# Performance work log

Hardware: AMD Instinct MI355X
Metric: run time of the kernel (lower is better)

The kernel has to match this reference:

```python
import jax, jax.numpy as jnp
import numpy as np
from jax import lax

NUM_CLASSES = 3
NORMALIZE = True
INF = 1e6  # finite 'infinity'; INF**2 = 1e12 is safely representable in fp32


def _dist_along_axis0(m):
    """Per-column 1D distance to nearest True along axis 0. m: [H,W] bool -> [H,W] float."""
    W = m.shape[1]
    init = jnp.full((W,), INF, dtype=jnp.float32)

    def step(carry, row):
        d = jnp.where(row, 0.0, carry + 1.0)
        return d, d

    _, fwd = lax.scan(step, init, m)
    _, bwd = lax.scan(step, init, m[::-1])
    return jnp.minimum(fwd, bwd[::-1])


def _dist_to_set(m):
    """Exact Euclidean distance to nearest True pixel (separable EDT). m: [H,W] bool."""
    W = m.shape[1]
    g = _dist_along_axis0(m)  # [H,W]: min |i-i'| with m[i',j]
    j = jnp.arange(W, dtype=jnp.float32)
    offs = (j[:, None] - j[None, :]) ** 2  # [W_out, W_src]
    # D2[i,j] = min_k g[i,k]^2 + (j-k)^2  (exact 2D squared EDT)
    d2 = jnp.min(g[:, None, :] ** 2 + offs[None, :, :], axis=-1)  # [H,W]
    return jnp.sqrt(d2)


def _sdf(mask):
    """Signed distance map bg_dist - fg_dist for one binary mask [H,W], matching onehot_to_sdf."""
    fg_dist = _dist_to_set(~mask)  # scipy edt(fg): distance to nearest zero of fg
    bg_dist = _dist_to_set(mask)   # scipy edt(1-fg): distance to nearest fg pixel
    if NORMALIZE:
        fg_dist = fg_dist / jnp.maximum(jnp.max(fg_dist), 1e-12)
        bg_dist = bg_dist / jnp.maximum(jnp.max(bg_dist), 1e-12)
    return jnp.where(jnp.any(mask), bg_dist - fg_dist, 0.0)


def _distance_maps(targets):
    onehot = jax.nn.one_hot(targets, NUM_CLASSES, axis=-1) > 0.5  # [B,H,W,C] bool
    masks = jnp.moveaxis(onehot, -1, 1)  # [B,C,H,W]
    B, C, H, W = masks.shape
    maps = lax.map(_sdf, masks.reshape(B * C, H, W))  # sequential: bounds peak memory
    return maps.reshape(B, C, H, W)


def setup_inputs() -> dict:
    key = jax.random.key(0)
    k1, k2 = jax.random.split(key)
    logits = jax.random.normal(k1, (8, 3, 384, 384), dtype=jnp.float32)
    targets = jax.random.randint(k2, (8, 384, 384), 0, 3, dtype=jnp.int32)
    return {"logits": logits, "targets": targets}


def reference(logits, targets):
    probs = jax.nn.softmax(logits, axis=1)              # [B,C,H,W]
    dist_maps = _distance_maps(targets)                  # [B,C,H,W]
    per_class = jnp.mean(probs * dist_maps, axis=(0, 2, 3))  # mean over b,h,w
    return jnp.mean(per_class)  # class_weights=None -> plain mean over classes
```

## Files before the change

### kernel.cpp

```cpp
#include <hip/hip_runtime.h>

typedef unsigned long long u64;
typedef unsigned short u16;

#define HH 384
#define WW 384
#define BB 8
#define CC 3
#define NMASK (BB*CC)
#define PLANE (HH*WW)
#define NW 6
#define ROWS_PG 4
#define GROUPS 96
#define CHUNK 4
#define INF_F 1.0e6f


template <int CTRL>
__device__ __forceinline__ float dpp_mov(float v) {
    return __int_as_float(__builtin_amdgcn_update_dpp(
        0, __float_as_int(v), CTRL, 0xf, 0xf, true));
}
__device__ __forceinline__ float wave_sum64(float v) {
    v += dpp_mov<0x111>(v);
    v += dpp_mov<0x112>(v);
    v += dpp_mov<0x114>(v);
    v += dpp_mov<0x118>(v);
    v += dpp_mov<0x142>(v);
    v += dpp_mov<0x143>(v);
    return v;
}
__device__ __forceinline__ float wave_max64(float v) {
    v = fmaxf(v, dpp_mov<0x111>(v));
    v = fmaxf(v, dpp_mov<0x112>(v));
    v = fmaxf(v, dpp_mov<0x114>(v));
    v = fmaxf(v, dpp_mov<0x118>(v));
    v = fmaxf(v, dpp_mov<0x142>(v));
    v = fmaxf(v, dpp_mov<0x143>(v));
    return v;
}

__global__ __launch_bounds__(WW) void buildbm(const int* __restrict__ targets,
                                              u16* __restrict__ bm16) {
    int b = blockIdx.x, w = blockIdx.y, q = blockIdx.z;
    int j = threadIdx.x;
    const int* tg = targets + (size_t)b * PLANE + (w * 64 + q * 16) * WW + j;
    int t[16];
#pragma unroll
    for (int r = 0; r < 16; ++r) t[r] = tg[r * WW];
    unsigned m0 = 0, m1 = 0, m2 = 0;
#pragma unroll
    for (int r = 0; r < 16; ++r) {
        unsigned bit = 1u << r;
        m0 |= (t[r] == 0) ? bit : 0u;
        m1 |= (t[r] == 1) ? bit : 0u;
        m2 |= (t[r] == 2) ? bit : 0u;
    }
    size_t base = (((size_t)b * CC) * NW + w) * WW + j;
    bm16[base * 4 + q] = (u16)m0;
    bm16[(base + (size_t)NW * WW) * 4 + q] = (u16)m1;
    bm16[(base + 2 * (size_t)NW * WW) * 4 + q] = (u16)m2;
}

__global__ __launch_bounds__(WW, 5) void edt4w(const u64* __restrict__ bm,
                                               const float* __restrict__ logits,
                                               float* __restrict__ out12) {
    __shared__ __align__(16) float g2s[ROWS_PG][CC][WW];
    __shared__ float red[12][WW / 64];
    int g = blockIdx.x, b = blockIdx.y;
    int j = threadIdx.x;
    int i0 = g * ROWS_PG;
    int w = i0 >> 6;
    int wbase = w << 6;

    u64 wb[CC][NW];
#pragma unroll
    for (int c = 0; c < CC; ++c)
#pragma unroll
        for (int wq = 0; wq < NW; ++wq)
            wb[c][wq] = bm[(((size_t)b * CC + c) * NW + wq) * WW + j];

    const float* lg = logits + ((size_t)b * CC * HH + i0) * WW + j;
    float lv[ROWS_PG][CC];
#pragma unroll
    for (int rl = 0; rl < ROWS_PG; ++rl) {
        lv[rl][0] = lg[rl * WW];
        lv[rl][1] = lg[PLANE + rl * WW];
        lv[rl][2] = lg[2 * PLANE + rl * WW];
    }

    u64 word[CC];
    int P[CC], N[CC];
#pragma unroll
    for (int c = 0; c < CC; ++c) {
        int p = -1, n = -1;
#pragma unroll
        for (int wq = 0; wq < NW; ++wq)
            if (wq < w && wb[c][wq]) p = wq * 64 + 63 - __builtin_clzll(wb[c][wq] | 1ull);
#pragma unroll
        for (int wq = NW - 1; wq >= 0; --wq)
            if (wq > w && wb[c][wq]) n = wq * 64 + (int)__builtin_ctzll(wb[c][wq] | 0x8000000000000000ull);
        P[c] = p; N[c] = n;
        u64 wd = wb[c][0];
#pragma unroll
        for (int wq = 1; wq < NW; ++wq) wd = (w == wq) ? wb[c][wq] : wd;
        word[c] = wd;
    }

    u64 lowmask = ((1ull << (i0 & 63)) << 1) - 1ull;
#pragma unroll
    for (int rl = 0; rl < ROWS_PG; ++rl) {
        int i = i0 + rl;
        u64 himask = ~(lowmask >> 1);
#pragma unroll
        for (int c = 0; c < CC; ++c) {
            u64 lo = word[c] & lowmask;
            int last = lo ? (wbase + 63 - __builtin_clzll(lo | 1ull)) : P[c];
            u64 hi = word[c] & himask;
            int next = hi ? (wbase + (int)__builtin_ctzll(hi | 0x8000000000000000ull)) : N[c];
            float fwd = (last >= 0) ? (float)(i - last) : (INF_F + (float)(i + 1));
            float bwd = (next >= 0) ? (float)(next - i) : (INF_F + (float)(HH - i));
            float gc = fminf(fwd, bwd);
            g2s[rl][c][j] = gc * gc;
        }
        lowmask = (lowmask << 1) | 1ull;
    }
    __syncthreads();

    int basek = (j - 4) & ~3;
    if (basek < 0) basek = 0;
    if (basek > WW - 12) basek = WW - 12;
    float df0 = (float)(basek - j);

    float Sb0 = 0.f, Sb1 = 0.f, Sb2 = 0.f, Sf0 = 0.f, Sf1 = 0.f, Sf2 = 0.f;
    float Mb0 = 0.f, Mb1 = 0.f, Mb2 = 0.f, Mf0 = 0.f, Mf1 = 0.f, Mf2 = 0.f;
#pragma unroll
    for (int rl = 0; rl < ROWS_PG; ++rl) {
        int bi = (i0 + rl) & 63;
        float l0 = lv[rl][0], l1 = lv[rl][1], l2 = lv[rl][2];
        float mx = fmaxf(l0, fmaxf(l1, l2));
        float x0 = __expf(l0 - mx), x1 = __expf(l1 - mx), x2 = __expf(l2 - mx);
        float rs = __fdividef(1.0f, x0 + x1 + x2);
        float pr0 = x0 * rs, pr1 = x1 * rs, pr2 = x2 * rs;

        float d[CC];
#pragma unroll
        for (int c = 0; c < CC; ++c) {
            const float* g2 = g2s[rl][c];
            float4 W0 = *(const float4*)(g2 + basek);
            float4 W1 = *(const float4*)(g2 + basek + 4);
            float4 W2 = *(const float4*)(g2 + basek + 8);
            float df = df0;
            float mn;
            mn =           fmaf(df, df, W0.x);  df += 1.f;
            mn = fminf(mn, fmaf(df, df, W0.y)); df += 1.f;
            mn = fminf(mn, fmaf(df, df, W0.z)); df += 1.f;
            mn = fminf(mn, fmaf(df, df, W0.w)); df += 1.f;
            mn = fminf(mn, fmaf(df, df, W1.x)); df += 1.f;
            mn = fminf(mn, fmaf(df, df, W1.y)); df += 1.f;
            mn = fminf(mn, fmaf(df, df, W1.z)); df += 1.f;
            mn = fminf(mn, fmaf(df, df, W1.w)); df += 1.f;
            mn = fminf(mn, fmaf(df, df, W2.x)); df += 1.f;
            mn = fminf(mn, fmaf(df, df, W2.y)); df += 1.f;
            mn = fminf(mn, fmaf(df, df, W2.z)); df += 1.f;
            mn = fminf(mn, fmaf(df, df, W2.w));
            if (mn > 25.f) {
                for (int r0 = 5; r0 < WW; r0 += CHUNK) {
                    float r0sq = (float)(r0 * r0);
                    if (r0sq >= mn) break;
                    float cl[CHUNK], cr[CHUNK];
#pragma unroll
                    for (int u = 0; u < CHUNK; ++u) {
                        int r = r0 + u;
                        int kl = j - r; kl = (kl < 0) ? 0 : kl;
                        int kr = j + r; kr = (kr > WW - 1) ? WW - 1 : kr;
                        cl[u] = g2[kl];
                        cr[u] = g2[kr];
                    }
#pragma unroll
                    for (int u = 0; u < CHUNK; ++u) {
                        float rr = (float)((r0 + u) * (r0 + u));
                        mn = fminf(mn, fminf(rr + cl[u], rr + cr[u]));
                    }
                }
            }
            d[c] = sqrtf(mn);
        }
        float f0 = ((word[0] >> bi) & 1ull) ? fminf(d[1], d[2]) : 0.f;
        float f1 = ((word[1] >> bi) & 1ull) ? fminf(d[0], d[2]) : 0.f;
        float f2 = ((word[2] >> bi) & 1ull) ? fminf(d[0], d[1]) : 0.f;

        Sb0 += pr0 * d[0]; Sb1 += pr1 * d[1]; Sb2 += pr2 * d[2];
        Sf0 += pr0 * f0;   Sf1 += pr1 * f1;   Sf2 += pr2 * f2;
        Mb0 = fmaxf(Mb0, d[0]); Mb1 = fmaxf(Mb1, d[1]); Mb2 = fmaxf(Mb2, d[2]);
        Mf0 = fmaxf(Mf0, f0);   Mf1 = fmaxf(Mf1, f1);   Mf2 = fmaxf(Mf2, f2);
    }

    float acc[12] = {Sb0, Sf0, Mb0, Mf0, Sb1, Sf1, Mb1, Mf1, Sb2, Sf2, Mb2, Mf2};
    int lane = j & 63, wid = j >> 6;
#pragma unroll
    for (int a = 0; a < 12; ++a) {
        bool ismax = (a & 2) != 0;
        float v = ismax ? wave_max64(acc[a]) : wave_sum64(acc[a]);
        if (lane == 63) red[a][wid] = v;
    }
    __syncthreads();
    if (j < 12) {
        int c = j >> 2, k = j & 3;
        bool ismax = (k & 2) != 0;
        float v = red[j][0];
#pragma unroll
        for (int t = 1; t < WW / 64; ++t)
            v = ismax ? fmaxf(v, red[j][t]) : (v + red[j][t]);
        out12[((size_t)(b * CC + c) * 4 + k) * GROUPS + g] = v;
    }
}

__global__ __launch_bounds__(WW) void final_k(const float* __restrict__ out12,
                                              float* __restrict__ out) {
    __shared__ float contrib[NMASK];
    int t = threadIdx.x;
    int m = t >> 4, l = t & 15;
    const float* pm = out12 + (size_t)m * 4 * GROUPS;
    float t0[6], t1[6], t2[6], t3[6];
#pragma unroll
    for (int q = 0; q < 6; ++q) {
        int gg = q * 16 + l;
        t0[q] = pm[0 * GROUPS + gg];
        t1[q] = pm[1 * GROUPS + gg];
        t2[q] = pm[2 * GROUPS + gg];
        t3[q] = pm[3 * GROUPS + gg];
    }
    float sb = 0.f, sf = 0.f, mb = 0.f, mf = 0.f;
#pragma unroll
    for (int q = 0; q < 6; ++q) {
        sb += t0[q]; sf += t1[q];
        mb = fmaxf(mb, t2[q]); mf = fmaxf(mf, t3[q]);
    }
#pragma unroll
    for (int off = 8; off > 0; off >>= 1) {
        sb += __shfl_down(sb, off, 16);
        sf += __shfl_down(sf, off, 16);
        mb = fmaxf(mb, __shfl_down(mb, off, 16));
        mf = fmaxf(mf, __shfl_down(mf, off, 16));
    }
    if (l == 0) {
        float cv = 0.f;
        if (mb <= 1000.0f)
            cv = sb / fmaxf(mb, 1e-12f) - sf / fmaxf(mf, 1e-12f);
        contrib[m] = cv;
    }
    __syncthreads();
    if (t == 0) {
        float tot = 0.f;
        for (int mk = 0; mk < NMASK; ++mk) tot += contrib[mk];
        out[0] = tot / (float)((size_t)BB * CC * PLANE);
    }
}

extern "C" void kernel_launch(void* const* d_in, const int* in_sizes, int n_in,
                              void* d_out, int out_size, void* d_ws, size_t ws_size,
                              hipStream_t stream) {
    const float* logits = (const float*)d_in[0];
    const int* targets = (const int*)d_in[1];
    float* out = (float*)d_out;

    u64* bm = (u64*)d_ws;
    float* out12 = (float*)(bm + (size_t)BB * CC * NW * WW);

    {
        dim3 grid(BB, NW, 4);
        buildbm<<<grid, WW, 0, stream>>>(targets, (u16*)bm);
    }
    {
        dim3 grid(GROUPS, BB);
        edt4w<<<grid, WW, 0, stream>>>(bm, logits, out12);
    }
    final_k<<<1, WW, 0, stream>>>(out12, out);
}
```

Before: 79.02 us.

## Precompute per-word first/last set-bit summaries to cut EDT bitmask loads

buildbm now builds full 64-row bitmask words in a single pass. It also writes a compact per-column auxiliary table holding the first and last set bit of each 64-row word. The EDT kernel then loads only its own word plus one 16-byte aux vector per class, instead of all six u64 words per class. This cuts global loads and register pressure, so the occupancy hint is raised from 5 to 8. In exchange, buildbm has fewer blocks and each thread holds 64 loaded values, which may lower that kernel's parallelism.

Result: no change. 79.65 us (+0.8%).

```diff
diff --git a/kernel.cpp b/kernel.cpp
--- a/kernel.cpp
+++ b/kernel.cpp
@@ -13,6 +13,7 @@
 #define ROWS_PG 4
 #define GROUPS 96
 #define CHUNK 4
+#define AUXW 8
 #define INF_F 1.0e6f
 
 
@@ -40,29 +41,38 @@
     return v;
 }
 
-__global__ __launch_bounds__(WW) void buildbm(const int* __restrict__ targets,
-                                              u16* __restrict__ bm16) {
-    int b = blockIdx.x, w = blockIdx.y, q = blockIdx.z;
+__global__ __launch_bounds__(WW, 4) void buildbm(const int* __restrict__ targets,
+                                                 u64* __restrict__ bm,
+                                                 u16* __restrict__ aux) {
+    int b = blockIdx.x, w = blockIdx.y;
     int j = threadIdx.x;
-    const int* tg = targets + (size_t)b * PLANE + (w * 64 + q * 16) * WW + j;
-    int t[16];
-#pragma unroll
-    for (int r = 0; r < 16; ++r) t[r] = tg[r * WW];
-    unsigned m0 = 0, m1 = 0, m2 = 0;
-#pragma unroll
-    for (int r = 0; r < 16; ++r) {
-        unsigned bit = 1u << r;
-        m0 |= (t[r] == 0) ? bit : 0u;
-        m1 |= (t[r] == 1) ? bit : 0u;
-        m2 |= (t[r] == 2) ? bit : 0u;
+    const int* tg = targets + (size_t)b * PLANE + (w * 64) * WW + j;
+    int t[64];
+#pragma unroll
+    for (int r = 0; r < 64; ++r) t[r] = tg[r * WW];
+    u64 m0 = 0, m1 = 0, m2 = 0;
+#pragma unroll
+    for (int r = 0; r < 64; ++r) {
+        u64 bit = 1ull << r;
+        m0 |= (t[r] == 0) ? bit : 0ull;
+        m1 |= (t[r] == 1) ? bit : 0ull;
+        m2 |= (t[r] == 2) ? bit : 0ull;
     }
     size_t base = (((size_t)b * CC) * NW + w) * WW + j;
-    bm16[base * 4 + q] = (u16)m0;
-    bm16[(base + (size_t)NW * WW) * 4 + q] = (u16)m1;
-    bm16[(base + 2 * (size_t)NW * WW) * 4 + q] = (u16)m2;
-}
-
-__global__ __launch_bounds__(WW, 5) void edt4w(const u64* __restrict__ bm,
+    bm[base] = m0;
+    bm[base + (size_t)NW * WW] = m1;
+    bm[base + 2 * (size_t)NW * WW] = m2;
+    u16 a0 = m0 ? (u16)(((63 - __builtin_clzll(m0)) << 8) | __builtin_ctzll(m0)) : (u16)0xFFFF;
+    u16 a1 = m1 ? (u16)(((63 - __builtin_clzll(m1)) << 8) | __builtin_ctzll(m1)) : (u16)0xFFFF;
+    u16 a2 = m2 ? (u16)(((63 - __builtin_clzll(m2)) << 8) | __builtin_ctzll(m2)) : (u16)0xFFFF;
+    size_t abase = (((size_t)b * CC) * WW + j) * AUXW + w;
+    aux[abase] = a0;
+    aux[abase + (size_t)WW * AUXW] = a1;
+    aux[abase + 2 * (size_t)WW * AUXW] = a2;
+}
+
+__global__ __launch_bounds__(WW, 8) void edt4w(const u64* __restrict__ bm,
+                                               const u16* __restrict__ aux,
                                                const float* __restrict__ logits,
                                                float* __restrict__ out12) {
     __shared__ __align__(16) float g2s[ROWS_PG][CC][WW];
@@ -73,13 +83,14 @@
     int w = i0 >> 6;
     int wbase = w << 6;
 
-    u64 wb[CC][NW];
+    u64 word[CC];
 #pragma unroll
     for (int c = 0; c < CC; ++c)
-#pragma unroll
-        for (int wq = 0; wq < NW; ++wq)
-            wb[c][wq] = bm[(((size_t)b * CC + c) * NW + wq) * WW + j];
-
+        word[c] = bm[(((size_t)b * CC + c) * NW + w) * WW + j];
+    uint4 ax[CC];
+#pragma unroll
+    for (int c = 0; c < CC; ++c)
+        ax[c] = *(const uint4*)(aux + (((size_t)b * CC + c) * WW + j) * AUXW);
     const float* lg = logits + ((size_t)b * CC * HH + i0) * WW + j;
     float lv[ROWS_PG][CC];
 #pragma unroll
@@ -89,22 +100,21 @@
         lv[rl][2] = lg[2 * PLANE + rl * WW];
     }
 
-    u64 word[CC];
     int P[CC], N[CC];
 #pragma unroll
     for (int c = 0; c < CC; ++c) {
+        unsigned e0 = ax[c].x & 0xFFFFu, e1 = ax[c].x >> 16;
+        unsigned e2 = ax[c].y & 0xFFFFu, e3 = ax[c].y >> 16;
+        unsigned e4 = ax[c].z & 0xFFFFu, e5 = ax[c].z >> 16;
+        unsigned e[NW] = {e0, e1, e2, e3, e4, e5};
         int p = -1, n = -1;
 #pragma unroll
         for (int wq = 0; wq < NW; ++wq)
-            if (wq < w && wb[c][wq]) p = wq * 64 + 63 - __builtin_clzll(wb[c][wq] | 1ull);
+            if (wq < w && e[wq] != 0xFFFFu) p = wq * 64 + (int)(e[wq] >> 8);
 #pragma unroll
         for (int wq = NW - 1; wq >= 0; --wq)
-            if (wq > w && wb[c][wq]) n = wq * 64 + (int)__builtin_ctzll(wb[c][wq] | 0x8000000000000000ull);
+            if (wq > w && e[wq] != 0xFFFFu) n = wq * 64 + (int)(e[wq] & 0xFFu);
         P[c] = p; N[c] = n;
-        u64 wd = wb[c][0];
-#pragma unroll
-        for (int wq = 1; wq < NW; ++wq) wd = (w == wq) ? wb[c][wq] : wd;
-        word[c] = wd;
     }
 
     u64 lowmask = ((1ull << (i0 & 63)) << 1) - 1ull;
@@ -164,7 +174,7 @@
             mn = fminf(mn, fmaf(df, df, W2.y)); df += 1.f;
             mn = fminf(mn, fmaf(df, df, W2.z)); df += 1.f;
             mn = fminf(mn, fmaf(df, df, W2.w));
-            if (mn > 25.f) {
+            if (__builtin_expect(mn > 25.f, 0)) {
                 for (int r0 = 5; r0 < WW; r0 += CHUNK) {
                     float r0sq = (float)(r0 * r0);
                     if (r0sq >= mn) break;
@@ -266,15 +276,16 @@
     float* out = (float*)d_out;
 
     u64* bm = (u64*)d_ws;
-    float* out12 = (float*)(bm + (size_t)BB * CC * NW * WW);
+    u16* aux = (u16*)(bm + (size_t)BB * CC * NW * WW);
+    float* out12 = (float*)(aux + (size_t)BB * CC * WW * AUXW);
 
     {
-        dim3 grid(BB, NW, 4);
-        buildbm<<<grid, WW, 0, stream>>>(targets, (u16*)bm);
+        dim3 grid(BB, NW);
+        buildbm<<<grid, WW, 0, stream>>>(targets, bm, aux);
     }
     {
         dim3 grid(GROUPS, BB);
-        edt4w<<<grid, WW, 0, stream>>>(bm, logits, out12);
+        edt4w<<<grid, WW, 0, stream>>>(bm, aux, logits, out12);
     }
     final_k<<<1, WW, 0, stream>>>(out12, out);
 }
```
